# Performance work log

Hardware: AMD Instinct MI355X
Metric: run time of the kernel (lower is better)

Reference implementation:

```python
import jax, jax.numpy as jnp
import numpy as np

N_NODES = 50000
N_EDGES = 800000
N_RELS = 16
D = 128


def _rgcn_layer(h, W, b, loop_w, gate_w, src, dst, rel, norm, apply_relu, n_nodes):
    # Transform all node features by every relation weight once: [R, N, D_out].
    # Equivalent to DGL bmm_maybe_select's per-edge W[rel] bmm, but avoids an
    # [E, D, D] gather of weights.
    h_all = jnp.einsum('nd,rde->rne', h, W)
    msg = h_all[rel, src]                                    # [E, D_out]
    msg = msg * norm                                         # edge norm scaling
    gate_logit = jnp.einsum('nd,rd->rn', h, gate_w[..., 0])  # [R, N]
    gate = jax.nn.sigmoid(gate_logit[rel, src])[:, None]     # [E, 1]
    msg = msg * gate
    agg = jax.ops.segment_sum(msg, dst, num_segments=n_nodes)  # fn.sum -> dst
    out = agg + b + h @ loop_w                               # bias + self loop
    if apply_relu:
        out = jax.nn.relu(out)
    return out  # dropout is identity in eval mode


def setup_inputs() -> dict:
    key = jax.random.key(0)
    ks = jax.random.split(key, 12)
    gain = float(np.sqrt(2.0))  # relu gain (xavier-ish scale; values arbitrary)
    def xav(k, shape):
        fan = shape[-2] + shape[-1]
        s = gain * np.sqrt(6.0 / fan)
        return jax.random.uniform(k, shape, jnp.float32, -s, s)
    return {
        'h': jax.random.normal(ks[0], (N_NODES, D), jnp.float32),
        'norm': jax.random.uniform(ks[1], (N_EDGES, 1), jnp.float32),
        'weight0': xav(ks[2], (N_RELS, D, D)),
        'bias0': jnp.zeros((D,), jnp.float32),
        'loop_w0': xav(ks[3], (D, D)),
        'gate_w0': xav(ks[4], (N_RELS, D, 1)),
        'weight1': xav(ks[5], (N_RELS, D, D)),
        'bias1': jnp.zeros((D,), jnp.float32),
        'loop_w1': xav(ks[6], (D, D)),
        'gate_w1': xav(ks[7], (N_RELS, D, 1)),
        'src': jax.random.randint(ks[8], (N_EDGES,), 0, N_NODES, jnp.int32),
        'dst': jax.random.randint(ks[9], (N_EDGES,), 0, N_NODES, jnp.int32),
        'rel_type': jax.random.randint(ks[10], (N_EDGES,), 0, N_RELS, jnp.int32),
    }


def reference(h, norm, weight0, bias0, loop_w0, gate_w0,
              weight1, bias1, loop_w1, gate_w1, src, dst, rel_type):
    n_nodes = h.shape[0]
    # Layer 0: activation=relu (idx < num_hidden_layers - 1)
    h = _rgcn_layer(h, weight0, bias0, loop_w0, gate_w0, src, dst, rel_type,
                    norm, True, n_nodes)
    # Layer 1: no activation
    h = _rgcn_layer(h, weight1, bias1, loop_w1, gate_w1, src, dst, rel_type,
                    norm, False, n_nodes)
    return h
```

## Files before the change

### kernel.cpp

```cpp
#include <hip/hip_runtime.h>
#include <hip/hip_bf16.h>
#include <stdint.h>

#define NN 50000
#define NE 800000
#define NR 16
#define SCAN_NB ((NN + 255) / 256)

typedef unsigned short u16;
typedef unsigned int u32;

typedef __bf16 bf16x8 __attribute__((ext_vector_type(8)));
typedef float f32x4 __attribute__((ext_vector_type(4)));

__device__ __forceinline__ u16 f2bf(float f) {
  u32 u = __float_as_uint(f);
  u = u + 0x7FFFu + ((u >> 16) & 1u);
  return (u16)(u >> 16);
}

__global__ void hist_kernel(const int* __restrict__ dst, int* __restrict__ counts) {
  int e = blockIdx.x * 256 + threadIdx.x;
  if (e < NE) atomicAdd(&counts[dst[e]], 1);
}

__global__ void scan_partial(const int* __restrict__ counts, int* __restrict__ bsum) {
  __shared__ int buf[256];
  int t = threadIdx.x;
  int i = blockIdx.x * 256 + t;
  int v = (i < NN) ? counts[i] : 0;
  buf[t] = v;
  __syncthreads();
  for (int off = 1; off < 256; off <<= 1) {
    int x = buf[t];
    int y = (t >= off) ? buf[t - off] : 0;
    __syncthreads();
    buf[t] = x + y;
    __syncthreads();
  }
  if (t == 255) bsum[blockIdx.x] = buf[255];
}

__global__ void scan_blocksums(const int* __restrict__ bsum, int* __restrict__ boff,
                               int* __restrict__ starts) {
  __shared__ int buf[256];
  int t = threadIdx.x;
  buf[t] = (t < SCAN_NB) ? bsum[t] : 0;
  __syncthreads();
  for (int off = 1; off < 256; off <<= 1) {
    int x = buf[t];
    int y = (t >= off) ? buf[t - off] : 0;
    __syncthreads();
    buf[t] = x + y;
    __syncthreads();
  }
  if (t < SCAN_NB) boff[t] = buf[t] - bsum[t];
  if (t == 255) starts[NN] = buf[255];
}

__global__ void scan_final(const int* __restrict__ counts, const int* __restrict__ boff,
                           int* __restrict__ starts, int* __restrict__ cursor) {
  __shared__ int buf[256];
  int t = threadIdx.x;
  int i = blockIdx.x * 256 + t;
  int v = (i < NN) ? counts[i] : 0;
  buf[t] = v;
  __syncthreads();
  for (int off = 1; off < 256; off <<= 1) {
    int x = buf[t];
    int y = (t >= off) ? buf[t - off] : 0;
    __syncthreads();
    buf[t] = x + y;
    __syncthreads();
  }
  int s = boff[blockIdx.x] + buf[t] - v;
  if (i < NN) {
    starts[i] = s;
    cursor[i] = s;
  }
}

__global__ void scatter_kernel(const int* __restrict__ src, const int* __restrict__ dst,
                               const int* __restrict__ rel, const float* __restrict__ norm,
                               int* __restrict__ cursor, u32* __restrict__ ssr,
                               float* __restrict__ snorm) {
  int e = blockIdx.x * 256 + threadIdx.x;
  if (e < NE) {
    int d = dst[e];
    int pos = atomicAdd(&cursor[d], 1);
    ssr[pos] = ((u32)rel[e] << 16) | (u32)src[e];
    snorm[pos] = norm[e];
  }
}

__global__ void convert_wt(const float* __restrict__ w0, const float* __restrict__ lw0,
                           const float* __restrict__ w1, const float* __restrict__ lw1,
                           u16* __restrict__ Wt) {
  int m = blockIdx.y;
  int idx = blockIdx.x * 256 + threadIdx.x;
  int d = idx >> 7, k = idx & 127;
  const float* s;
  if (m < 16) s = w0 + (size_t)m * 16384;
  else if (m == 16) s = lw0;
  else if (m < 33) s = w1 + (size_t)(m - 17) * 16384;
  else s = lw1;
  Wt[(size_t)m * 16384 + idx] = f2bf(s[k * 128 + d]);
}

__global__ void gates_kernel(const float* __restrict__ h, const float* __restrict__ gw,
                             float* __restrict__ gates) {
  __shared__ float hs[16 * 132];
  __shared__ float gws[16 * 132];
  int t = threadIdx.x;
  int n0 = blockIdx.x * 16;
#pragma unroll
  for (int i = 0; i < 2; ++i) {
    int f = t + 256 * i;
    int row = f >> 5, c4 = (f & 31) * 4;
    *(float4*)&hs[row * 132 + c4] = *(const float4*)&h[(size_t)(n0 + row) * 128 + c4];
    *(float4*)&gws[row * 132 + c4] = *(const float4*)&gw[row * 128 + c4];
  }
  __syncthreads();
  int nl = t >> 4, r = t & 15;
  float s = 0.f;
#pragma unroll 8
  for (int k = 0; k < 128; ++k) s += hs[nl * 132 + k] * gws[r * 132 + k];
  gates[r * NN + n0 + nl] = 1.f / (1.f + __expf(-s));
}

template <bool WF32>
__global__ __launch_bounds__(256, 2)
void transform_kernel(const float* __restrict__ h, const u16* __restrict__ Wt,
                      int mat_cnt, u16* __restrict__ tmp,
                      float* __restrict__ fout, const float* __restrict__ bias) {
  __shared__ u16 As[128 * 136];
  __shared__ u16 Bs[128 * 136];
  int t = threadIdx.x;
  int n0 = blockIdx.x * 128;
#pragma unroll
  for (int i = 0; i < 16; ++i) {
    int f = t + 256 * i;
    int row = f >> 5, c4 = (f & 31) * 4;
    int n = n0 + row;
    float4 v = make_float4(0.f, 0.f, 0.f, 0.f);
    if (n < NN) v = *(const float4*)&h[(size_t)n * 128 + c4];
    ushort4 u;
    u.x = f2bf(v.x); u.y = f2bf(v.y); u.z = f2bf(v.z); u.w = f2bf(v.w);
    *(ushort4*)&As[row * 136 + c4] = u;
  }
  int wave = t >> 6, lane = t & 63;
  int wr = (wave >> 1) * 64, wc = (wave & 1) * 64;
  int mrow = lane & 15, quad = lane >> 4;
  for (int m = 0; m < mat_cnt; ++m) {
    __syncthreads();
#pragma unroll
    for (int i = 0; i < 8; ++i) {
      int u8 = t + 256 * i;
      int row = u8 >> 4, c8 = (u8 & 15) * 8;
      *(uint4*)&Bs[row * 136 + c8] = *(const uint4*)&Wt[(size_t)m * 16384 + row * 128 + c8];
    }
    __syncthreads();
    f32x4 acc[4][4];
#pragma unroll
    for (int i = 0; i < 4; ++i)
#pragma unroll
      for (int j = 0; j < 4; ++j) acc[i][j] = (f32x4){0.f, 0.f, 0.f, 0.f};
#pragma unroll
    for (int kk = 0; kk < 4; ++kk) {
      int k0 = kk * 32 + quad * 8;
      bf16x8 a[4], b[4];
#pragma unroll
      for (int i = 0; i < 4; ++i) a[i] = *(const bf16x8*)&As[(wr + i * 16 + mrow) * 136 + k0];
#pragma unroll
      for (int j = 0; j < 4; ++j) b[j] = *(const bf16x8*)&Bs[(wc + j * 16 + mrow) * 136 + k0];
#pragma unroll
      for (int i = 0; i < 4; ++i)
#pragma unroll
        for (int j = 0; j < 4; ++j)
          acc[i][j] = __builtin_amdgcn_mfma_f32_16x16x32_bf16(a[i], b[j], acc[i][j], 0, 0, 0);
    }
#pragma unroll
    for (int i = 0; i < 4; ++i) {
#pragma unroll
      for (int r = 0; r < 4; ++r) {
        int row = wr + i * 16 + quad * 4 + r;
        int n = n0 + row;
        if (n < NN) {
#pragma unroll
          for (int j = 0; j < 4; ++j) {
            int col = wc + j * 16 + mrow;
            float v = acc[i][j][r];
            if (WF32) fout[(size_t)n * 128 + col] = v + bias[col];
            else tmp[((size_t)m * NN + n) * 128 + col] = f2bf(v);
          }
        }
      }
    }
  }
}

__global__ __launch_bounds__(256)
void aggregate_kernel(const u32* __restrict__ tmp, const u32* __restrict__ ssr,
                      const float* __restrict__ snorm, const float* __restrict__ gates,
                      const int* __restrict__ starts, float* __restrict__ hout,
                      int mat_lo, int mat_cnt, int relu) {
  int wave = threadIdx.x >> 6, lane = threadIdx.x & 63;
  int v = blockIdx.x * 4 + wave;
  if (v >= NN) return;
  int s = starts[v], e = starts[v + 1];
  float a0 = 0.f, a1 = 0.f;
#pragma unroll 4
  for (int j = s; j < e; ++j) {
    u32 pk = ssr[j];
    int rel = (int)(pk >> 16);
    u32 rl = (u32)(rel - mat_lo);
    if (rl < (u32)mat_cnt) {
      int sn = (int)(pk & 0xFFFFu);
      float scl = snorm[j] * gates[rel * NN + sn];
      u32 w = tmp[((size_t)rl * NN + sn) * 64 + lane];
      a0 += scl * __uint_as_float(w << 16);
      a1 += scl * __uint_as_float(w & 0xFFFF0000u);
    }
  }
  float2* ho = (float2*)&hout[(size_t)v * 128 + lane * 2];
  float2 base = *ho;
  float o0 = base.x + a0, o1 = base.y + a1;
  if (relu) { o0 = fmaxf(o0, 0.f); o1 = fmaxf(o1, 0.f); }
  *ho = make_float2(o0, o1);
}

static void run_layer(const float* hin, const u16* Wt, int wt_base,
                      const float* gw, const float* bias, float* hout,
                      u16* tmp, const u32* ssr, const float* snorm,
                      float* gates, const int* starts, int mats_per_chunk,
                      int relu, hipStream_t stream) {
  gates_kernel<<<NN / 16, 256, 0, stream>>>(hin, gw, gates);
  transform_kernel<true><<<(NN + 127) / 128, 256, 0, stream>>>(
      hin, Wt + (size_t)(wt_base + 16) * 16384, 1, nullptr, hout, bias);
  for (int lo = 0; lo < NR; lo += mats_per_chunk) {
    int cnt = NR - lo < mats_per_chunk ? NR - lo : mats_per_chunk;
    transform_kernel<false><<<(NN + 127) / 128, 256, 0, stream>>>(
        hin, Wt + (size_t)(wt_base + lo) * 16384, cnt, tmp, nullptr, nullptr);
    int last = (lo + cnt >= NR);
    aggregate_kernel<<<(NN + 3) / 4, 256, 0, stream>>>(
        (const u32*)tmp, ssr, snorm, gates, starts, hout, lo, cnt, relu && last);
  }
}

extern "C" void kernel_launch(void* const* d_in, const int* in_sizes, int n_in,
                              void* d_out, int out_size, void* d_ws, size_t ws_size,
                              hipStream_t stream) {
  const float* h0   = (const float*)d_in[0];
  const float* norm = (const float*)d_in[1];
  const float* w0   = (const float*)d_in[2];
  const float* b0   = (const float*)d_in[3];
  const float* lw0  = (const float*)d_in[4];
  const float* gw0  = (const float*)d_in[5];
  const float* w1   = (const float*)d_in[6];
  const float* b1   = (const float*)d_in[7];
  const float* lw1  = (const float*)d_in[8];
  const float* gw1  = (const float*)d_in[9];
  const int*   src  = (const int*)d_in[10];
  const int*   dst  = (const int*)d_in[11];
  const int*   rel  = (const int*)d_in[12];
  float* out = (float*)d_out;

  char* p = (char*)d_ws;
  auto alloc = [&](size_t bytes) -> void* {
    void* q = (void*)p;
    p += (bytes + 255) & ~(size_t)255;
    return q;
  };
  u16*   Wt     = (u16*)alloc((size_t)34 * 16384 * 2);
  float* gates  = (float*)alloc((size_t)NR * NN * 4);
  float* h1     = (float*)alloc((size_t)NN * 128 * 4);
  int*   counts = (int*)alloc((size_t)NN * 4);
  int*   cursor = (int*)alloc((size_t)NN * 4);
  int*   starts = (int*)alloc((size_t)(NN + 1) * 4);
  int*   bsum   = (int*)alloc((size_t)256 * 4);
  int*   boff   = (int*)alloc((size_t)256 * 4);
  u32*   ssr    = (u32*)alloc((size_t)NE * 4);
  float* snorm  = (float*)alloc((size_t)NE * 4);
  size_t used = (size_t)(p - (char*)d_ws);
  size_t per_mat = (size_t)NN * 128 * 2;
  int mats = (int)((ws_size > used ? ws_size - used : 0) / per_mat);
  if (mats > NR) mats = NR;
  if (mats < 1) mats = 1;
  u16* tmp = (u16*)alloc((size_t)mats * per_mat);

  hipMemsetAsync(counts, 0, (size_t)NN * 4, stream);
  hist_kernel<<<NE / 256, 256, 0, stream>>>(dst, counts);
  scan_partial<<<SCAN_NB, 256, 0, stream>>>(counts, bsum);
  scan_blocksums<<<1, 256, 0, stream>>>(bsum, boff, starts);
  scan_final<<<SCAN_NB, 256, 0, stream>>>(counts, boff, starts, cursor);
  scatter_kernel<<<NE / 256, 256, 0, stream>>>(src, dst, rel, norm, cursor, ssr, snorm);
  convert_wt<<<dim3(64, 34), 256, 0, stream>>>(w0, lw0, w1, lw1, Wt);

  run_layer(h0, Wt, 0,  gw0, b0, h1,  tmp, ssr, snorm, gates, starts, mats, 1, stream);
  run_layer(h1, Wt, 17, gw1, b1, out, tmp, ssr, snorm, gates, starts, mats, 0, stream);
}
```

Baseline: 551.9 us.

## Fold gates into transform epilogue, pack edge data, batch aggregate gathers

Converts node features to bf16 once per layer and has the transform kernel read them directly. It multiplies each transformed row by its per-relation gate before storing, so aggregation no longer gathers gates. Edge source/relation and norm are packed into one 8-byte record. The transform grid is split across relations via blockIdx.y for more blocks, and the full-relation aggregate path issues eight independent gathers per iteration. The extra conversion kernel and buffer cost a little extra bandwidth, and the gate is now applied before bf16 rounding.

```diff
diff --git a/kernel.cpp b/kernel.cpp
--- a/kernel.cpp
+++ b/kernel.cpp
@@ -6,6 +6,7 @@
 #define NE 800000
 #define NR 16
 #define SCAN_NB ((NN + 255) / 256)
+#define NTILES ((NN + 127) / 128)
 
 typedef unsigned short u16;
 typedef unsigned int u32;
@@ -82,14 +83,12 @@
 
 __global__ void scatter_kernel(const int* __restrict__ src, const int* __restrict__ dst,
                                const int* __restrict__ rel, const float* __restrict__ norm,
-                               int* __restrict__ cursor, u32* __restrict__ ssr,
-                               float* __restrict__ snorm) {
+                               int* __restrict__ cursor, uint2* __restrict__ esd) {
   int e = blockIdx.x * 256 + threadIdx.x;
   if (e < NE) {
     int d = dst[e];
     int pos = atomicAdd(&cursor[d], 1);
-    ssr[pos] = ((u32)rel[e] << 16) | (u32)src[e];
-    snorm[pos] = norm[e];
+    esd[pos] = make_uint2(((u32)rel[e] << 16) | (u32)src[e], __float_as_uint(norm[e]));
   }
 }
 
@@ -107,6 +106,14 @@
   Wt[(size_t)m * 16384 + idx] = f2bf(s[k * 128 + d]);
 }
 
+__global__ void hconv_kernel(const float* __restrict__ h, u16* __restrict__ hbf) {
+  int i = blockIdx.x * 256 + threadIdx.x;
+  float4 v = ((const float4*)h)[i];
+  ushort4 u;
+  u.x = f2bf(v.x); u.y = f2bf(v.y); u.z = f2bf(v.z); u.w = f2bf(v.w);
+  ((ushort4*)hbf)[i] = u;
+}
+
 __global__ void gates_kernel(const float* __restrict__ h, const float* __restrict__ gw,
                              float* __restrict__ gates) {
   __shared__ float hs[16 * 132];
@@ -130,28 +137,30 @@
 
 template <bool WF32>
 __global__ __launch_bounds__(256, 2)
-void transform_kernel(const float* __restrict__ h, const u16* __restrict__ Wt,
-                      int mat_cnt, u16* __restrict__ tmp,
-                      float* __restrict__ fout, const float* __restrict__ bias) {
+void transform_kernel(const u16* __restrict__ hbf, const u16* __restrict__ Wt,
+                      int cnt, int CM, const float* __restrict__ gate_base,
+                      u16* __restrict__ tmp, float* __restrict__ fout,
+                      const float* __restrict__ bias) {
   __shared__ u16 As[128 * 136];
   __shared__ u16 Bs[128 * 136];
+  __shared__ float gs[128];
   int t = threadIdx.x;
   int n0 = blockIdx.x * 128;
 #pragma unroll
-  for (int i = 0; i < 16; ++i) {
-    int f = t + 256 * i;
-    int row = f >> 5, c4 = (f & 31) * 4;
+  for (int i = 0; i < 8; ++i) {
+    int u8 = t + 256 * i;
+    int row = u8 >> 4, c8 = (u8 & 15) * 8;
     int n = n0 + row;
-    float4 v = make_float4(0.f, 0.f, 0.f, 0.f);
-    if (n < NN) v = *(const float4*)&h[(size_t)n * 128 + c4];
-    ushort4 u;
-    u.x = f2bf(v.x); u.y = f2bf(v.y); u.z = f2bf(v.z); u.w = f2bf(v.w);
-    *(ushort4*)&As[row * 136 + c4] = u;
+    uint4 v = make_uint4(0, 0, 0, 0);
+    if (n < NN) v = *(const uint4*)&hbf[(size_t)n * 128 + c8];
+    *(uint4*)&As[row * 136 + c8] = v;
   }
   int wave = t >> 6, lane = t & 63;
   int wr = (wave >> 1) * 64, wc = (wave & 1) * 64;
   int mrow = lane & 15, quad = lane >> 4;
-  for (int m = 0; m < mat_cnt; ++m) {
+  int m0 = blockIdx.y * CM;
+  int m1 = m0 + CM < cnt ? m0 + CM : cnt;
+  for (int m = m0; m < m1; ++m) {
     __syncthreads();
 #pragma unroll
     for (int i = 0; i < 8; ++i) {
@@ -159,6 +168,10 @@
       int row = u8 >> 4, c8 = (u8 & 15) * 8;
       *(uint4*)&Bs[row * 136 + c8] = *(const uint4*)&Wt[(size_t)m * 16384 + row * 128 + c8];
     }
+    if (!WF32 && t < 128) {
+      int n = n0 + t;
+      gs[t] = (n < NN) ? gate_base[(size_t)m * NN + n] : 0.f;
+    }
     __syncthreads();
     f32x4 acc[4][4];
 #pragma unroll
@@ -186,12 +199,13 @@
         int row = wr + i * 16 + quad * 4 + r;
         int n = n0 + row;
         if (n < NN) {
+          float g = WF32 ? 0.f : gs[row];
 #pragma unroll
           for (int j = 0; j < 4; ++j) {
             int col = wc + j * 16 + mrow;
             float v = acc[i][j][r];
             if (WF32) fout[(size_t)n * 128 + col] = v + bias[col];
-            else tmp[((size_t)m * NN + n) * 128 + col] = f2bf(v);
+            else tmp[((size_t)m * NN + n) * 128 + col] = f2bf(v * g);
           }
         }
       }
@@ -199,9 +213,9 @@
   }
 }
 
+template <bool FULL>
 __global__ __launch_bounds__(256)
-void aggregate_kernel(const u32* __restrict__ tmp, const u32* __restrict__ ssr,
-                      const float* __restrict__ snorm, const float* __restrict__ gates,
+void aggregate_kernel(const u32* __restrict__ tmp, const uint2* __restrict__ esd,
                       const int* __restrict__ starts, float* __restrict__ hout,
                       int mat_lo, int mat_cnt, int relu) {
   int wave = threadIdx.x >> 6, lane = threadIdx.x & 63;
@@ -209,41 +223,69 @@
   if (v >= NN) return;
   int s = starts[v], e = starts[v + 1];
   float a0 = 0.f, a1 = 0.f;
-#pragma unroll 4
-  for (int j = s; j < e; ++j) {
-    u32 pk = ssr[j];
-    int rel = (int)(pk >> 16);
+  int j = s;
+  if (FULL) {
+    for (; j + 8 <= e; j += 8) {
+      uint2 p[8];
+      u32 w[8];
+      float sc[8];
+#pragma unroll
+      for (int i = 0; i < 8; ++i) p[i] = esd[j + i];
+#pragma unroll
+      for (int i = 0; i < 8; ++i) {
+        u32 rs = p[i].x;
+        u32 off = ((rs >> 16) * (u32)NN + (rs & 0xFFFFu)) * 64u + (u32)lane;
+        w[i] = tmp[off];
+        sc[i] = __uint_as_float(p[i].y);
+      }
+#pragma unroll
+      for (int i = 0; i < 8; ++i) {
+        a0 = fmaf(sc[i], __uint_as_float(w[i] << 16), a0);
+        a1 = fmaf(sc[i], __uint_as_float(w[i] & 0xFFFF0000u), a1);
+      }
+    }
+  }
+  for (; j < e; ++j) {
+    uint2 p = esd[j];
+    int rel = (int)(p.x >> 16);
     u32 rl = (u32)(rel - mat_lo);
-    if (rl < (u32)mat_cnt) {
-      int sn = (int)(pk & 0xFFFFu);
-      float scl = snorm[j] * gates[rel * NN + sn];
-      u32 w = tmp[((size_t)rl * NN + sn) * 64 + lane];
-      a0 += scl * __uint_as_float(w << 16);
-      a1 += scl * __uint_as_float(w & 0xFFFF0000u);
+    if (FULL || rl < (u32)mat_cnt) {
+      u32 off = (rl * (u32)NN + (p.x & 0xFFFFu)) * 64u + (u32)lane;
+      float sc = __uint_as_float(p.y);
+      u32 w = tmp[off];
+      a0 = fmaf(sc, __uint_as_float(w << 16), a0);
+      a1 = fmaf(sc, __uint_as_float(w & 0xFFFF0000u), a1);
     }
   }
   float2* ho = (float2*)&hout[(size_t)v * 128 + lane * 2];
-  float2 base = *ho;
-  float o0 = base.x + a0, o1 = base.y + a1;
+  float2 b = *ho;
+  float o0 = b.x + a0, o1 = b.y + a1;
   if (relu) { o0 = fmaxf(o0, 0.f); o1 = fmaxf(o1, 0.f); }
   *ho = make_float2(o0, o1);
 }
 
-static void run_layer(const float* hin, const u16* Wt, int wt_base,
+static void run_layer(const float* hin, u16* hbf, const u16* Wt, int wt_base,
                       const float* gw, const float* bias, float* hout,
-                      u16* tmp, const u32* ssr, const float* snorm,
-                      float* gates, const int* starts, int mats_per_chunk,
-                      int relu, hipStream_t stream) {
+                      u16* tmp, const uint2* esd, float* gates, const int* starts,
+                      int mats_per_chunk, int relu, hipStream_t stream) {
+  hconv_kernel<<<NN * 32 / 256, 256, 0, stream>>>(hin, hbf);
   gates_kernel<<<NN / 16, 256, 0, stream>>>(hin, gw, gates);
-  transform_kernel<true><<<(NN + 127) / 128, 256, 0, stream>>>(
-      hin, Wt + (size_t)(wt_base + 16) * 16384, 1, nullptr, hout, bias);
+  transform_kernel<true><<<dim3(NTILES, 1), 256, 0, stream>>>(
+      hbf, Wt + (size_t)(wt_base + 16) * 16384, 1, 1, nullptr, nullptr, hout, bias);
   for (int lo = 0; lo < NR; lo += mats_per_chunk) {
     int cnt = NR - lo < mats_per_chunk ? NR - lo : mats_per_chunk;
-    transform_kernel<false><<<(NN + 127) / 128, 256, 0, stream>>>(
-        hin, Wt + (size_t)(wt_base + lo) * 16384, cnt, tmp, nullptr, nullptr);
+    const int CM = 2;
+    int G = (cnt + CM - 1) / CM;
+    transform_kernel<false><<<dim3(NTILES, G), 256, 0, stream>>>(
+        hbf, Wt + (size_t)(wt_base + lo) * 16384, cnt, CM, gates + (size_t)lo * NN,
+        tmp, nullptr, nullptr);
     int last = (lo + cnt >= NR);
-    aggregate_kernel<<<(NN + 3) / 4, 256, 0, stream>>>(
-        (const u32*)tmp, ssr, snorm, gates, starts, hout, lo, cnt, relu && last);
+    if (cnt == NR)
+      aggregate_kernel<true><<<(NN + 3) / 4, 256, 0, stream>>>(
+          (const u32*)tmp, esd, starts, hout, 0, NR, relu && last);
+    else
+      aggregate_kernel<false><<<(NN + 3) / 4, 256, 0, stream>>>(
+          (const u32*)tmp, esd, starts, hout, lo, cnt, relu && last);
   }
 }
 
@@ -274,13 +316,13 @@
   u16*   Wt     = (u16*)alloc((size_t)34 * 16384 * 2);
   float* gates  = (float*)alloc((size_t)NR * NN * 4);
   float* h1     = (float*)alloc((size_t)NN * 128 * 4);
+  u16*   hbf    = (u16*)alloc((size_t)NN * 128 * 2);
   int*   counts = (int*)alloc((size_t)NN * 4);
   int*   cursor = (int*)alloc((size_t)NN * 4);
   int*   starts = (int*)alloc((size_t)(NN + 1) * 4);
   int*   bsum   = (int*)alloc((size_t)256 * 4);
   int*   boff   = (int*)alloc((size_t)256 * 4);
-  u32*   ssr    = (u32*)alloc((size_t)NE * 4);
-  float* snorm  = (float*)alloc((size_t)NE * 4);
+  uint2* esd    = (uint2*)alloc((size_t)NE * 8);
   size_t used = (size_t)(p - (char*)d_ws);
   size_t per_mat = (size_t)NN * 128 * 2;
   int mats = (int)((ws_size > used ? ws_size - used : 0) / per_mat);
@@ -293,9 +335,9 @@
   scan_partial<<<SCAN_NB, 256, 0, stream>>>(counts, bsum);
   scan_blocksums<<<1, 256, 0, stream>>>(bsum, boff, starts);
   scan_final<<<SCAN_NB, 256, 0, stream>>>(counts, boff, starts, cursor);
-  scatter_kernel<<<NE / 256, 256, 0, stream>>>(src, dst, rel, norm, cursor, ssr, snorm);
+  scatter_kernel<<<NE / 256, 256, 0, stream>>>(src, dst, rel, norm, cursor, esd);
   convert_wt<<<dim3(64, 34), 256, 0, stream>>>(w0, lw0, w1, lw1, Wt);
 
-  run_layer(h0, Wt, 0,  gw0, b0, h1,  tmp, ssr, snorm, gates, starts, mats, 1, stream);
-  run_layer(h1, Wt, 17, gw1, b1, out, tmp, ssr, snorm, gates, starts, mats, 0, stream);
-}
+  run_layer(h0, hbf, Wt, 0,  gw0, b0, h1,  tmp, esd, gates, starts, mats, 1, stream);
+  run_layer(h1, hbf, Wt, 17, gw1, b1, out, tmp, esd, gates, starts, mats, 0, stream);
+}
```

New measurement: 520.0 us. 1.06x faster.
